# Performance work log

Measured on AMD Instinct MI355X. Metric: run time of the kernel, lower is better.

The kernel has to match this reference:

```python
import jax, jax.numpy as jnp
import numpy as np

SEQ_LENGTH = 8192
P_DIM = 128  # number of landmarks


def setup_inputs() -> dict:
    key = jax.random.key(0)
    kq, kk, kv = jax.random.split(key, 3)
    shape = (4, 16, SEQ_LENGTH, 64)  # [b, h, n, d]
    return {
        "q": jax.random.normal(kq, shape, dtype=jnp.float32),
        "k": jax.random.normal(kk, shape, dtype=jnp.float32),
        "v": jax.random.normal(kv, shape, dtype=jnp.float32),
    }


def _landmarks(x, p_dim, seq_length):
    # mean-pool groups of size l = ceil(seq/p_dim) into p_dim landmarks,
    # left-padding with zeros when seq % p_dim != 0 (matches torch F.pad)
    b, h, n, d = x.shape
    l = int(np.ceil(seq_length / p_dim))
    remainder = seq_length % p_dim
    if remainder > 0:
        padding = p_dim - remainder
        x = jnp.pad(x, ((0, 0), (0, 0), (padding, 0), (0, 0)))
    return x.reshape(b, h, p_dim, l, d).mean(axis=3)  # [b, h, m, d]


def reference(q, k, v):
    q = q / (q.shape[-1] ** 0.5)
    q_land = _landmarks(q, P_DIM, SEQ_LENGTH)  # [b, h, m, d]
    k_land = _landmarks(k, P_DIM, SEQ_LENGTH)  # [b, h, m, d]

    # F: queries attend to key-landmarks  [b, h, n, m]
    F = jax.nn.softmax(jnp.einsum('bhid,bhjd->bhij', q, k_land), axis=-1)
    # A: pinv of landmark-landmark attention  [b, h, m, m]
    A = jnp.linalg.pinv(jax.nn.softmax(jnp.einsum('bhid,bhjd->bhij', q_land, k_land), axis=-1))
    # B: query-landmarks attend to keys  [b, h, m, n]
    B = jax.nn.softmax(jnp.einsum('bhid,bhjd->bhij', q_land, k), axis=-1)

    # (F @ A) @ (B @ v) == F @ (A @ (B @ v)); use cheap association
    return F @ (A @ (B @ v))  # [b, h, n, d]
```

## Files before the change

### kernel.cpp

```cpp
#include <hip/hip_runtime.h>
#include <hip/hip_bf16.h>
#include <math.h>

#define BH 64
#define NSEQ 8192
#define DHEAD 64
#define M 128
#define LGRP 64
#define NCB 4
#define KPB (NSEQ / NCB)
#define TILE 64
#define NTILE (KPB / TILE)
#define NSWEEP 8
#define NROUND 127
#define RCOND 1.52587890625e-4

__global__ __launch_bounds__(64) void lm_kernel(const float* __restrict__ q,
                                                const float* __restrict__ k,
                                                double* __restrict__ ql64,
                                                double* __restrict__ kl64,
                                                float* __restrict__ qlf32,
                                                float* __restrict__ klf32) {
    int idx = blockIdx.x;
    int tensor = idx >> 13;
    int g = idx & 8191;
    int head = g >> 7, m = g & 127;
    int d = threadIdx.x;
    const float* src = tensor ? k : q;
    const float* base = src + ((size_t)head * NSEQ + (size_t)m * LGRP) * DHEAD + d;
    double s = 0.0;
    #pragma unroll 8
    for (int r = 0; r < LGRP; ++r) s += (double)base[(size_t)r * DHEAD];
    s *= (1.0 / LGRP);
    if (!tensor) s *= 0.125;
    size_t o = (size_t)head * M * DHEAD + (size_t)m * DHEAD + d;
    if (!tensor) { ql64[o] = s; qlf32[o] = (float)s; }
    else         { kl64[o] = s; klf32[o] = (float)s; }
}

__global__ __launch_bounds__(512) void s_kernel(const double* __restrict__ ql64,
                                                const double* __restrict__ kl64,
                                                double* __restrict__ Sg) {
    extern __shared__ double lds[];
    double* qlds = lds;
    double* klds = lds + M * DHEAD;
    int head = blockIdx.x;
    int t = threadIdx.x;
    const double2* qg = (const double2*)(ql64 + (size_t)head * M * DHEAD);
    const double2* kg = (const double2*)(kl64 + (size_t)head * M * DHEAD);
    for (int e = t; e < M * DHEAD / 2; e += 512) {
        ((double2*)qlds)[e] = qg[e];
        ((double2*)klds)[e] = kg[e];
    }
    __syncthreads();
    int tr = t >> 4, tc = t & 15;
    double acc[4][8];
    #pragma unroll
    for (int i = 0; i < 4; ++i)
        #pragma unroll
        for (int j = 0; j < 8; ++j) acc[i][j] = 0.0;
    for (int dc = 0; dc < DHEAD; dc += 4) {
        double qreg[4][4], kreg[8][4];
        #pragma unroll
        for (int i = 0; i < 4; ++i)
            #pragma unroll
            for (int d = 0; d < 4; ++d) qreg[i][d] = qlds[(4 * tr + i) * DHEAD + dc + d];
        #pragma unroll
        for (int j = 0; j < 8; ++j)
            #pragma unroll
            for (int d = 0; d < 4; ++d) kreg[j][d] = klds[(8 * tc + j) * DHEAD + dc + d];
        #pragma unroll
        for (int i = 0; i < 4; ++i)
            #pragma unroll
            for (int j = 0; j < 8; ++j)
                #pragma unroll
                for (int d = 0; d < 4; ++d) acc[i][j] += qreg[i][d] * kreg[j][d];
    }
    double* So = Sg + (size_t)head * M * M;
    #pragma unroll
    for (int i = 0; i < 4; ++i) {
        double mx = acc[i][0];
        #pragma unroll
        for (int j = 1; j < 8; ++j) mx = fmax(mx, acc[i][j]);
        mx = fmax(mx, __shfl_xor(mx, 1));
        mx = fmax(mx, __shfl_xor(mx, 2));
        mx = fmax(mx, __shfl_xor(mx, 4));
        mx = fmax(mx, __shfl_xor(mx, 8));
        double sum = 0.0;
        #pragma unroll
        for (int j = 0; j < 8; ++j) { acc[i][j] = exp(acc[i][j] - mx); sum += acc[i][j]; }
        sum += __shfl_xor(sum, 1); sum += __shfl_xor(sum, 2);
        sum += __shfl_xor(sum, 4); sum += __shfl_xor(sum, 8);
        double inv = 1.0 / sum;
        #pragma unroll
        for (int j = 0; j < 8; ++j)
            So[(size_t)(8 * tc + j) * M + 4 * tr + i] = acc[i][j] * inv;
    }
}

__global__ __launch_bounds__(512) void fused_kernel(const double* __restrict__ Sg,
                                                    double* __restrict__ Wcol,
                                                    const float* __restrict__ k,
                                                    const float* __restrict__ v,
                                                    const float* __restrict__ qlf32,
                                                    double* __restrict__ numd,
                                                    double* __restrict__ dend) {
    extern __shared__ double ldsd[];
    __shared__ double norms2[M];
    __shared__ double maxn2s;
    __shared__ int anyrot, done;
    int t = threadIdx.x;

    if (blockIdx.x < BH) {
        int head = blockIdx.x;
        double* G = ldsd;
        const double2* Sh2 = (const double2*)(Sg + (size_t)head * M * M);
        double2* G2 = (double2*)G;
        for (int e = t; e < M * 64; e += 512) {
            int col = e >> 6, rp = e & 63;
            G2[col * 65 + rp] = Sh2[e];
        }
        __syncthreads();
        {
            int col = t >> 2, qd = t & 3;
            double s = 0.0;
            #pragma unroll 8
            for (int x = qd * 32; x < qd * 32 + 32; ++x) { double vv = G[col * 130 + x]; s += vv * vv; }
            s += __shfl_xor(s, 1); s += __shfl_xor(s, 2);
            if (qd == 0) norms2[col] = s;
        }
        if (t == 0) { anyrot = 1; done = 0; }
        __syncthreads();
        int grp = t >> 3, s8 = t & 7;
        for (int sweep = 0; sweep < NSWEEP; ++sweep) {
            if (t < 64) {
                double mm = fmax(norms2[t], norms2[t + 64]);
                for (int off = 32; off > 0; off >>= 1) mm = fmax(mm, __shfl_down(mm, off));
                if (t == 0) {
                    maxn2s = mm;
                    done = (sweep > 0 && anyrot == 0);
                    anyrot = 0;
                }
            }
            __syncthreads();
            if (done) break;
            double kc = maxn2s * (RCOND * RCOND);
            for (int r = 0; r < NROUND; ++r) {
                int ca, cb;
                if (grp == 0) { ca = 127; cb = r; }
                else { ca = (r + grp) % 127; cb = (r + 127 - grp) % 127; }
                double na = norms2[ca], nb = norms2[cb];
                if (na + nb >= kc) {
                    double2* gA = (double2*)(G + ca * 130);
                    double2* gB = (double2*)(G + cb * 130);
                    double2 va[8], vb[8];
                    #pragma unroll
                    for (int j = 0; j < 8; ++j) va[j] = gA[j * 8 + s8];
                    #pragma unroll
                    for (int j = 0; j < 8; ++j) vb[j] = gB[j * 8 + s8];
                    double c = 0.0;
                    #pragma unroll
                    for (int j = 0; j < 8; ++j) c += va[j].x * vb[j].x + va[j].y * vb[j].y;
                    c += __shfl_xor(c, 1); c += __shfl_xor(c, 2); c += __shfl_xor(c, 4);
                    if (c * c > 1e-24 * na * nb) {
                        if (na > kc && nb > kc && c * c > 1e-12 * na * nb) anyrot = 1;
                        double zeta = (nb - na) / (2.0 * c);
                        double tt = (zeta >= 0.0 ? 1.0 : -1.0) / (fabs(zeta) + sqrt(1.0 + zeta * zeta));
                        double cs = 1.0 / sqrt(1.0 + tt * tt);
                        double sn = cs * tt;
                        #pragma unroll
                        for (int j = 0; j < 8; ++j) {
                            double nax = cs * va[j].x - sn * vb[j].x;
                            double nay = cs * va[j].y - sn * vb[j].y;
                            double nbx = sn * va[j].x + cs * vb[j].x;
                            double nby = sn * va[j].y + cs * vb[j].y;
                            gA[j * 8 + s8] = make_double2(nax, nay);
                            gB[j * 8 + s8] = make_double2(nbx, nby);
                        }
                        if (s8 == 0) {
                            norms2[ca] = fmax(na - tt * c, 0.0);
                            norms2[cb] = nb + tt * c;
                        }
                    }
                }
                __syncthreads();
            }
        }
        {
            int col = t >> 2, qd = t & 3;
            double s = 0.0;
            #pragma unroll 8
            for (int x = qd * 32; x < qd * 32 + 32; ++x) { double vv = G[col * 130 + x]; s += vv * vv; }
            s += __shfl_xor(s, 1); s += __shfl_xor(s, 2);
            if (qd == 0) norms2[col] = s;
        }
        __syncthreads();
        if (t < 64) {
            double mm = fmax(norms2[t], norms2[t + 64]);
            for (int off = 32; off > 0; off >>= 1) mm = fmax(mm, __shfl_down(mm, off));
            if (t == 0) maxn2s = mm;
        }
        __syncthreads();
        double cut2 = maxn2s * (RCOND * RCOND);
        for (int e = t; e < M * M; e += 512) {
            int cc = e >> 7, rr = e & 127;
            double n2 = norms2[cc];
            Wcol[(size_t)blockIdx.x * M * M + e] = (n2 > cut2) ? G[cc * 130 + rr] / n2 : 0.0;
        }
    } else {
        int bb = blockIdx.x - BH;
        int head = bb >> 2;
        int chunk = bb & 3;
        float* F = (float*)ldsd;
        float* qls = F;
        float* kls = F + 8704;
        float* vls = F + 13056;
        float* Zl  = F + 17408;
        {
            const float4* qg = (const float4*)(qlf32 + (size_t)head * M * DHEAD);
            for (int e = t; e < 2048; e += 512) {
                int m = e >> 4, dq = e & 15;
                *(float4*)&qls[m * 68 + dq * 4] = qg[e];
            }
        }
        int mb = t >> 4, lo = t & 15;
        double acc64[16];
        double den64[4];
        #pragma unroll
        for (int i = 0; i < 16; ++i) acc64[i] = 0.0;
        #pragma unroll
        for (int i = 0; i < 4; ++i) den64[i] = 0.0;
        size_t keybase = (size_t)head * NSEQ + (size_t)chunk * KPB;
        for (int tt = 0; tt < NTILE; ++tt) {
            __syncthreads();
            const float4* kg = (const float4*)(k + (keybase + tt * TILE) * DHEAD);
            const float4* vg = (const float4*)(v + (keybase + tt * TILE) * DHEAD);
            for (int e = t; e < 1024; e += 512) {
                int key = e >> 4, dq = e & 15;
                *(float4*)&kls[key * 68 + dq * 4] = kg[e];
                *(float4*)&vls[key * 68 + dq * 4] = vg[e];
            }
            __syncthreads();
            float z0[4], z1[4], z2[4], z3[4];
            #pragma unroll
            for (int j = 0; j < 4; ++j) { z0[j] = 0.f; z1[j] = 0.f; z2[j] = 0.f; z3[j] = 0.f; }
            for (int dc = 0; dc < DHEAD; dc += 4) {
                float4 qr[4], kr[4];
                #pragma unroll
                for (int i = 0; i < 4; ++i) qr[i] = *(const float4*)&qls[(mb * 4 + i) * 68 + dc];
                #pragma unroll
                for (int j = 0; j < 4; ++j) kr[j] = *(const float4*)&kls[(j * 16 + lo) * 68 + dc];
                #pragma unroll
                for (int j = 0; j < 4; ++j) {
                    z0[j] += qr[0].x * kr[j].x + qr[0].y * kr[j].y + qr[0].z * kr[j].z + qr[0].w * kr[j].w;
                    z1[j] += qr[1].x * kr[j].x + qr[1].y * kr[j].y + qr[1].z * kr[j].z + qr[1].w * kr[j].w;
                    z2[j] += qr[2].x * kr[j].x + qr[2].y * kr[j].y + qr[2].z * kr[j].z + qr[2].w * kr[j].w;
                    z3[j] += qr[3].x * kr[j].x + qr[3].y * kr[j].y + qr[3].z * kr[j].z + qr[3].w * kr[j].w;
                }
            }
            #pragma unroll
            for (int j = 0; j < 4; ++j) {
                float4 ej;
                ej.x = __expf(z0[j]); ej.y = __expf(z1[j]);
                ej.z = __expf(z2[j]); ej.w = __expf(z3[j]);
                *(float4*)&Zl[(j * 16 + lo) * 132 + mb * 4] = ej;
            }
            __syncthreads();
            float4 a32[4];
            #pragma unroll
            for (int i = 0; i < 4; ++i) a32[i] = make_float4(0.f, 0.f, 0.f, 0.f);
            float den32[4] = {0.f, 0.f, 0.f, 0.f};
            for (int key = 0; key < TILE; ++key) {
                float4 vv = *(const float4*)&vls[key * 68 + lo * 4];
                float4 ee = *(const float4*)&Zl[key * 132 + mb * 4];
                a32[0].x += ee.x * vv.x; a32[0].y += ee.x * vv.y; a32[0].z += ee.x * vv.z; a32[0].w += ee.x * vv.w;
                a32[1].x += ee.y * vv.x; a32[1].y += ee.y * vv.y; a32[1].z += ee.y * vv.z; a32[1].w += ee.y * vv.w;
                a32[2].x += ee.z * vv.x; a32[2].y += ee.z * vv.y; a32[2].z += ee.z * vv.z; a32[2].w += ee.z * vv.w;
                a32[3].x += ee.w * vv.x; a32[3].y += ee.w * vv.y; a32[3].z += ee.w * vv.z; a32[3].w += ee.w * vv.w;
                if (lo == 0) { den32[0] += ee.x; den32[1] += ee.y; den32[2] += ee.z; den32[3] += ee.w; }
            }
            #pragma unroll
            for (int i = 0; i < 4; ++i) {
                acc64[i * 4 + 0] += (double)a32[i].x;
                acc64[i * 4 + 1] += (double)a32[i].y;
                acc64[i * 4 + 2] += (double)a32[i].z;
                acc64[i * 4 + 3] += (double)a32[i].w;
            }
            if (lo == 0) {
                #pragma unroll
                for (int i = 0; i < 4; ++i) den64[i] += (double)den32[i];
            }
        }
        #pragma unroll
        for (int i = 0; i < 4; ++i) {
            size_t ob = (((size_t)head * NCB + chunk) * M + mb * 4 + i) * DHEAD + lo * 4;
            *(double2*)&numd[ob]     = make_double2(acc64[i * 4 + 0], acc64[i * 4 + 1]);
            *(double2*)&numd[ob + 2] = make_double2(acc64[i * 4 + 2], acc64[i * 4 + 3]);
        }
        if (lo == 0) {
            #pragma unroll
            for (int i = 0; i < 4; ++i)
                dend[((size_t)head * NCB + chunk) * M + mb * 4 + i] = den64[i];
        }
    }
}

__global__ __launch_bounds__(512) void apply_kernel(const double* __restrict__ numd,
                                                    const double* __restrict__ dend,
                                                    const double* __restrict__ Wcol,
                                                    const double* __restrict__ Sg,
                                                    float* __restrict__ ABvf32) {
    extern __shared__ double lds[];
    double* A_ = lds;
    double* B_ = lds + M * 66;
    __shared__ double dsum[M];
    int head = blockIdx.x;
    int t = threadIdx.x;
    if (t < M) {
        double s = 0.0;
        #pragma unroll
        for (int c = 0; c < NCB; ++c) s += dend[((size_t)head * NCB + c) * M + t];
        dsum[t] = s;
    }
    __syncthreads();
    for (int e = t; e < M * DHEAD; e += 512) {
        int mm = e >> 6;
        double s = 0.0;
        #pragma unroll
        for (int c = 0; c < NCB; ++c) s += numd[((size_t)head * NCB + c) * (M * DHEAD) + e];
        A_[mm * 66 + (e & 63)] = s / dsum[mm];
    }
    __syncthreads();
    int i = t >> 3, qd = t & 7;
    const double* Wb = Wcol + (size_t)head * M * M;
    const double* Sb = Sg + (size_t)head * M * M;
    {
        double a0[8], a1[8];
        #pragma unroll
        for (int d = 0; d < 8; ++d) { a0[d] = 0.0; a1[d] = 0.0; }
        for (int r = 0; r < M; ++r) {
            double m0 = Wb[(size_t)i * M + r];
            double m1 = Wb[(size_t)(i + 64) * M + r];
            #pragma unroll
            for (int d = 0; d < 8; ++d) {
                double xv = A_[r * 66 + qd * 8 + d];
                a0[d] += m0 * xv; a1[d] += m1 * xv;
            }
        }
        #pragma unroll
        for (int d = 0; d < 8; ++d) {
            B_[i * 66 + qd * 8 + d] = a0[d];
            B_[(i + 64) * 66 + qd * 8 + d] = a1[d];
        }
    }
    __syncthreads();
    {
        double a0[8], a1[8];
        #pragma unroll
        for (int d = 0; d < 8; ++d) { a0[d] = 0.0; a1[d] = 0.0; }
        for (int r = 0; r < M; ++r) {
            double m0 = Wb[(size_t)r * M + i];
            double m1 = Wb[(size_t)r * M + i + 64];
            #pragma unroll
            for (int d = 0; d < 8; ++d) {
                double xv = B_[r * 66 + qd * 8 + d];
                a0[d] += m0 * xv; a1[d] += m1 * xv;
            }
        }
        #pragma unroll
        for (int d = 0; d < 8; ++d) {
            A_[i * 66 + qd * 8 + d] = a0[d];
            A_[(i + 64) * 66 + qd * 8 + d] = a1[d];
        }
    }
    __syncthreads();
    {
        double a0[8], a1[8];
        #pragma unroll
        for (int d = 0; d < 8; ++d) { a0[d] = 0.0; a1[d] = 0.0; }
        for (int r = 0; r < M; ++r) {
            double m0 = Sb[(size_t)i * M + r];
            double m1 = Sb[(size_t)(i + 64) * M + r];
            #pragma unroll
            for (int d = 0; d < 8; ++d) {
                double xv = A_[r * 66 + qd * 8 + d];
                a0[d] += m0 * xv; a1[d] += m1 * xv;
            }
        }
        float* ob = ABvf32 + (size_t)head * M * DHEAD;
        #pragma unroll
        for (int d = 0; d < 8; ++d) {
            ob[i * DHEAD + qd * 8 + d] = (float)a0[d];
            ob[(i + 64) * DHEAD + qd * 8 + d] = (float)a1[d];
        }
    }
}

__global__ __launch_bounds__(512) void out_kernel(const float* __restrict__ q,
                                                  const float* __restrict__ klf32,
                                                  const float* __restrict__ ABvf32,
                                                  float* __restrict__ out) {
    __shared__ float kls[M * DHEAD];
    __shared__ float avs[M * DHEAD];
    int head = blockIdx.x >> 4;
    int tile = blockIdx.x & 15;
    int t = threadIdx.x;
    for (int e = t; e < M * DHEAD; e += 512) {
        kls[e] = klf32[(size_t)head * M * DHEAD + e];
        avs[e] = ABvf32[(size_t)head * M * DHEAD + e];
    }
    __syncthreads();
    int rl = t >> 1, h = t & 1;
    size_t row0 = (size_t)head * NSEQ + (size_t)tile * 512 + rl;
    size_t row1 = row0 + 256;
    const float4* qr0 = (const float4*)(q + row0 * DHEAD + h * 32);
    const float4* qr1 = (const float4*)(q + row1 * DHEAD + h * 32);
    float4 qa[8], qb[8];
    #pragma unroll
    for (int c = 0; c < 8; ++c) {
        float4 x = qr0[c];
        x.x *= 0.125f; x.y *= 0.125f; x.z *= 0.125f; x.w *= 0.125f;
        qa[c] = x;
        float4 y = qr1[c];
        y.x *= 0.125f; y.y *= 0.125f; y.z *= 0.125f; y.w *= 0.125f;
        qb[c] = y;
    }
    float acc0[32], acc1[32];
    #pragma unroll
    for (int d = 0; d < 32; ++d) { acc0[d] = 0.f; acc1[d] = 0.f; }
    float d0 = 0.f, d1 = 0.f;
    for (int mm = 0; mm < M; ++mm) {
        const float4* kr = (const float4*)(kls + mm * DHEAD + h * 32);
        float z0 = 0.f, z1 = 0.f;
        #pragma unroll
        for (int c = 0; c < 8; ++c) {
            float4 kk = kr[c];
            z0 += qa[c].x * kk.x + qa[c].y * kk.y + qa[c].z * kk.z + qa[c].w * kk.w;
            z1 += qb[c].x * kk.x + qb[c].y * kk.y + qb[c].z * kk.z + qb[c].w * kk.w;
        }
        z0 += __shfl_xor(z0, 1);
        z1 += __shfl_xor(z1, 1);
        float e0 = __expf(z0), e1 = __expf(z1);
        d0 += e0; d1 += e1;
        const float4* ar = (const float4*)(avs + mm * DHEAD + h * 32);
        #pragma unroll
        for (int c = 0; c < 8; ++c) {
            float4 av = ar[c];
            acc0[4 * c]     += e0 * av.x; acc0[4 * c + 1] += e0 * av.y;
            acc0[4 * c + 2] += e0 * av.z; acc0[4 * c + 3] += e0 * av.w;
            acc1[4 * c]     += e1 * av.x; acc1[4 * c + 1] += e1 * av.y;
            acc1[4 * c + 2] += e1 * av.z; acc1[4 * c + 3] += e1 * av.w;
        }
    }
    float i0 = 1.f / d0, i1 = 1.f / d1;
    float* o0 = out + row0 * DHEAD + h * 32;
    float* o1 = out + row1 * DHEAD + h * 32;
    #pragma unroll
    for (int d = 0; d < 32; ++d) { o0[d] = acc0[d] * i0; o1[d] = acc1[d] * i1; }
}

extern "C" void kernel_launch(void* const* d_in, const int* in_sizes, int n_in,
                              void* d_out, int out_size, void* d_ws, size_t ws_size,
                              hipStream_t stream) {
    const float* q = (const float*)d_in[0];
    const float* k = (const float*)d_in[1];
    const float* v = (const float*)d_in[2];
    float* out = (float*)d_out;
    char* ws = (char*)d_ws;
    double* ql64  = (double*)(ws + 0);
    double* kl64  = (double*)(ws + 4194304);
    double* numd  = (double*)(ws + 0);
    double* dend  = (double*)(ws + 33554432);
    float*  qlf32 = (float*)(ws + 34078720);
    float*  klf32 = (float*)(ws + 36175872);
    double* Sg    = (double*)(ws + 38273024);
    double* Wcol  = (double*)(ws + 46661632);
    float*  ABvf32= (float*)(ws + 55050240);

    lm_kernel<<<16384, 64, 0, stream>>>(q, k, ql64, kl64, qlf32, klf32);
    s_kernel<<<BH, 512, 2 * M * DHEAD * 8, stream>>>(ql64, kl64, Sg);
    fused_kernel<<<BH + 256, 512, 133120, stream>>>(Sg, Wcol, k, v, qlf32, numd, dend);
    apply_kernel<<<BH, 512, 2 * M * 66 * 8, stream>>>(numd, dend, Wcol, Sg, ABvf32);
    out_kernel<<<BH * 16, 512, 0, stream>>>(q, klf32, ABvf32, out);
}
```

Before: 2.598 ms.

## Run one-sided Jacobi pinv in fp32 storage with column compaction after early sweeps

```diff
diff --git a/kernel.cpp b/kernel.cpp
--- a/kernel.cpp
+++ b/kernel.cpp
@@ -12,8 +12,9 @@
 #define TILE 64
 #define NTILE (KPB / TILE)
 #define NSWEEP 8
-#define NROUND 127
+#define COMPACT_SWEEP 3
 #define RCOND 1.52587890625e-4
+#define RC2 (RCOND * RCOND)
 
 __global__ __launch_bounds__(64) void lm_kernel(const float* __restrict__ q,
                                                 const float* __restrict__ k,
@@ -108,28 +109,27 @@
     extern __shared__ double ldsd[];
     __shared__ double norms2[M];
     __shared__ double maxn2s;
-    __shared__ int anyrot, done;
+    __shared__ int anyrot, done, ncols_s;
     int t = threadIdx.x;
 
     if (blockIdx.x < BH) {
         int head = blockIdx.x;
-        double* G = ldsd;
-        const double2* Sh2 = (const double2*)(Sg + (size_t)head * M * M);
-        double2* G2 = (double2*)G;
-        for (int e = t; e < M * 64; e += 512) {
-            int col = e >> 6, rp = e & 63;
-            G2[col * 65 + rp] = Sh2[e];
-        }
+        float* G32 = (float*)ldsd;
+        const double* Sh = Sg + (size_t)head * M * M;
+        for (int e = t; e < M * M; e += 512) {
+            int col = e >> 7, x = e & 127;
+            G32[col * 132 + x] = (float)Sh[e];
+        }
+        if (t == 0) { anyrot = 1; done = 0; ncols_s = M; }
         __syncthreads();
         {
             int col = t >> 2, qd = t & 3;
             double s = 0.0;
             #pragma unroll 8
-            for (int x = qd * 32; x < qd * 32 + 32; ++x) { double vv = G[col * 130 + x]; s += vv * vv; }
+            for (int x = qd * 32; x < qd * 32 + 32; ++x) { double vv = (double)G32[col * 132 + x]; s += vv * vv; }
             s += __shfl_xor(s, 1); s += __shfl_xor(s, 2);
             if (qd == 0) norms2[col] = s;
         }
-        if (t == 0) { anyrot = 1; done = 0; }
         __syncthreads();
         int grp = t >> 3, s8 = t & 7;
         for (int sweep = 0; sweep < NSWEEP; ++sweep) {
@@ -144,53 +144,95 @@
             }
             __syncthreads();
             if (done) break;
-            double kc = maxn2s * (RCOND * RCOND);
-            for (int r = 0; r < NROUND; ++r) {
-                int ca, cb;
-                if (grp == 0) { ca = 127; cb = r; }
-                else { ca = (r + grp) % 127; cb = (r + 127 - grp) % 127; }
-                double na = norms2[ca], nb = norms2[cb];
-                if (na + nb >= kc) {
-                    double2* gA = (double2*)(G + ca * 130);
-                    double2* gB = (double2*)(G + cb * 130);
-                    double2 va[8], vb[8];
-                    #pragma unroll
-                    for (int j = 0; j < 8; ++j) va[j] = gA[j * 8 + s8];
-                    #pragma unroll
-                    for (int j = 0; j < 8; ++j) vb[j] = gB[j * 8 + s8];
-                    double c = 0.0;
-                    #pragma unroll
-                    for (int j = 0; j < 8; ++j) c += va[j].x * vb[j].x + va[j].y * vb[j].y;
-                    c += __shfl_xor(c, 1); c += __shfl_xor(c, 2); c += __shfl_xor(c, 4);
-                    if (c * c > 1e-24 * na * nb) {
-                        if (na > kc && nb > kc && c * c > 1e-12 * na * nb) anyrot = 1;
-                        double zeta = (nb - na) / (2.0 * c);
-                        double tt = (zeta >= 0.0 ? 1.0 : -1.0) / (fabs(zeta) + sqrt(1.0 + zeta * zeta));
-                        double cs = 1.0 / sqrt(1.0 + tt * tt);
-                        double sn = cs * tt;
+            if (sweep == COMPACT_SWEEP) {
+                if (t < 64) {
+                    double kcc = maxn2s * RC2 * 0.25;
+                    int nk = 0;
+                    for (int c = 0; c < M; ++c) {
+                        double n2 = norms2[c];
+                        if (n2 > kcc) {
+                            if (nk != c) {
+                                float x0 = G32[c * 132 + t];
+                                float x1 = G32[c * 132 + 64 + t];
+                                G32[nk * 132 + t] = x0;
+                                G32[nk * 132 + 64 + t] = x1;
+                                if (t == 0) norms2[nk] = n2;
+                            }
+                            ++nk;
+                        }
+                    }
+                    if (nk & 1) {
+                        G32[nk * 132 + t] = 0.f;
+                        G32[nk * 132 + 64 + t] = 0.f;
+                        if (t == 0) norms2[nk] = 0.0;
+                        ++nk;
+                    }
+                    for (int c = nk + t; c < M; c += 64) norms2[c] = 0.0;
+                    if (t == 0) ncols_s = nk;
+                }
+                __syncthreads();
+            }
+            double kc = maxn2s * RC2;
+            int nc = ncols_s;
+            int half = nc >> 1, nm1 = nc - 1;
+            for (int r = 0; r < nm1; ++r) {
+                if (grp < half) {
+                    int ca, cb;
+                    if (grp == 0) { ca = nm1; cb = r; }
+                    else {
+                        int a = r + grp;        if (a >= nm1) a -= nm1;
+                        int b = r + nm1 - grp;  if (b >= nm1) b -= nm1;
+                        ca = a; cb = b;
+                    }
+                    double na = norms2[ca], nb = norms2[cb];
+                    if (na + nb >= kc) {
+                        float4* gA = (float4*)(G32 + ca * 132);
+                        float4* gB = (float4*)(G32 + cb * 132);
+                        float4 va[4], vb[4];
                         #pragma unroll
-                        for (int j = 0; j < 8; ++j) {
-                            double nax = cs * va[j].x - sn * vb[j].x;
-                            double nay = cs * va[j].y - sn * vb[j].y;
-                            double nbx = sn * va[j].x + cs * vb[j].x;
-                            double nby = sn * va[j].y + cs * vb[j].y;
-                            gA[j * 8 + s8] = make_double2(nax, nay);
-                            gB[j * 8 + s8] = make_double2(nbx, nby);
-                        }
-                        if (s8 == 0) {
-                            norms2[ca] = fmax(na - tt * c, 0.0);
-                            norms2[cb] = nb + tt * c;
+                        for (int j = 0; j < 4; ++j) va[j] = gA[j * 8 + s8];
+                        #pragma unroll
+                        for (int j = 0; j < 4; ++j) vb[j] = gB[j * 8 + s8];
+                        float c32 = 0.f;
+                        #pragma unroll
+                        for (int j = 0; j < 4; ++j)
+                            c32 += va[j].x * vb[j].x + va[j].y * vb[j].y
+                                 + va[j].z * vb[j].z + va[j].w * vb[j].w;
+                        c32 += __shfl_xor(c32, 1); c32 += __shfl_xor(c32, 2); c32 += __shfl_xor(c32, 4);
+                        double c = (double)c32;
+                        if (c * c > 1e-14 * na * nb) {
+                            if (na > kc && nb > kc && c * c > 1.6e-11 * na * nb) anyrot = 1;
+                            double zeta = (nb - na) / (2.0 * c);
+                            double tt = (zeta >= 0.0 ? 1.0 : -1.0) / (fabs(zeta) + sqrt(1.0 + zeta * zeta));
+                            double cs = 1.0 / sqrt(1.0 + tt * tt);
+                            double sn = cs * tt;
+                            float csf = (float)cs, snf = (float)sn;
+                            #pragma unroll
+                            for (int j = 0; j < 4; ++j) {
+                                float4 a = va[j], b = vb[j];
+                                gA[j * 8 + s8] = make_float4(csf * a.x - snf * b.x, csf * a.y - snf * b.y,
+                                                             csf * a.z - snf * b.z, csf * a.w - snf * b.w);
+                                gB[j * 8 + s8] = make_float4(snf * a.x + csf * b.x, snf * a.y + csf * b.y,
+                                                             snf * a.z + csf * b.z, snf * a.w + csf * b.w);
+                            }
+                            if (s8 == 0) {
+                                norms2[ca] = fmax(na - tt * c, 0.0);
+                                norms2[cb] = nb + tt * c;
+                            }
                         }
                     }
                 }
                 __syncthreads();
             }
         }
+        int nc = ncols_s;
         {
             int col = t >> 2, qd = t & 3;
             double s = 0.0;
-            #pragma unroll 8
-            for (int x = qd * 32; x < qd * 32 + 32; ++x) { double vv = G[col * 130 + x]; s += vv * vv; }
+            if (col < nc) {
+                #pragma unroll 8
+                for (int x = qd * 32; x < qd * 32 + 32; ++x) { double vv = (double)G32[col * 132 + x]; s += vv * vv; }
+            }
             s += __shfl_xor(s, 1); s += __shfl_xor(s, 2);
             if (qd == 0) norms2[col] = s;
         }
@@ -201,11 +243,12 @@
             if (t == 0) maxn2s = mm;
         }
         __syncthreads();
-        double cut2 = maxn2s * (RCOND * RCOND);
+        double cut2 = maxn2s * RC2;
         for (int e = t; e < M * M; e += 512) {
             int cc = e >> 7, rr = e & 127;
             double n2 = norms2[cc];
-            Wcol[(size_t)blockIdx.x * M * M + e] = (n2 > cut2) ? G[cc * 130 + rr] / n2 : 0.0;
+            Wcol[(size_t)head * M * M + e] =
+                (cc < nc && n2 > cut2) ? (double)G32[cc * 132 + rr] / n2 : 0.0;
         }
     } else {
         int bb = blockIdx.x - BH;
@@ -479,7 +522,7 @@
 
     lm_kernel<<<16384, 64, 0, stream>>>(q, k, ql64, kl64, qlf32, klf32);
     s_kernel<<<BH, 512, 2 * M * DHEAD * 8, stream>>>(ql64, kl64, Sg);
-    fused_kernel<<<BH + 256, 512, 133120, stream>>>(Sg, Wcol, k, v, qlf32, numd, dend);
+    fused_kernel<<<BH + 256, 512, 103424, stream>>>(Sg, Wcol, k, v, qlf32, numd, dend);
     apply_kernel<<<BH, 512, 2 * M * 66 * 8, stream>>>(numd, dend, Wcol, Sg, ABvf32);
     out_kernel<<<BH * 16, 512, 0, stream>>>(q, klf32, ABvf32, out);
 }
```

New measurement: 4.395 ms. +69.2%, slower.
